# Performance work log

Measured on AMD Instinct MI355X. Metric: run time of the kernel, lower is better.

## Reference

```python
import jax, jax.numpy as jnp
import numpy as np

N = 100000   # nodes
E = 1200000  # edges
D = 64       # input_features == hidden_features
L = 3        # num_layers
EPS = 1e-5   # BatchNorm1d eps
SLOPE = 0.2  # LeakyReLU negative slope


def setup_inputs() -> dict:
    key = jax.random.key(0)
    k_x, k_e, k_w = jax.random.split(key, 3)
    x = jax.random.normal(k_x, (N, D), dtype=jnp.float32)
    edge_index = jax.random.randint(k_e, (2, E), 0, N, dtype=jnp.int32)
    # Glorot-ish linear weights per layer, stacked [L, D, D]; bias zeros.
    Ws = jax.random.normal(k_w, (L, D, D), dtype=jnp.float32) / np.float32(np.sqrt(D))
    bs = jnp.zeros((L, D), dtype=jnp.float32)
    # BatchNorm affine params (training-mode batch statistics are used).
    gammas = jnp.ones((L, D), dtype=jnp.float32)
    betas = jnp.zeros((L, D), dtype=jnp.float32)
    return {"x": x, "edge_index": edge_index, "Ws": Ws, "bs": bs,
            "gammas": gammas, "betas": betas}


def reference(x, edge_index, Ws, bs, gammas, betas):
    src, dst = edge_index[0], edge_index[1]
    # GCN symmetric normalization with self-loops: deg = in-degree + 1
    deg = jax.ops.segment_sum(jnp.ones((E,), x.dtype), dst, num_segments=N) + 1.0
    dinv = jax.lax.rsqrt(deg)
    enorm = (dinv[src] * dinv[dst])[:, None]  # [E,1] edge norm
    snorm = (dinv * dinv)[:, None]            # [N,1] self-loop norm
    for l in range(L):
        xw = x @ Ws[l]                                        # [N,D]
        agg = (jax.ops.segment_sum(xw[src] * enorm, dst, num_segments=N)
               + xw * snorm + bs[l])                          # GCNConv output
        h = jnp.where(agg > 0, agg, SLOPE * agg)              # LeakyReLU(0.2)
        mu = h.mean(axis=0)
        var = h.var(axis=0)                                   # biased var (PyTorch BN)
        x = gammas[l] * (h - mu) * jax.lax.rsqrt(var + EPS) + betas[l]
    return x
```

## Files before the change

### kernel.cpp

```cpp
#include <hip/hip_runtime.h>

#define D 64
#define SLOPE 0.2f
#define BN_EPS 1e-5f
#define BSHIFT 9
#define BUCKET 512
#define CHUNK 8192

static __device__ __forceinline__ unsigned pk_bf16(float fx, float fy) {
    unsigned bx = __float_as_uint(fx);
    unsigned by = __float_as_uint(fy);
    bx = (bx + 0x7fffu + ((bx >> 16) & 1u)) >> 16;
    by = (by + 0x7fffu + ((by >> 16) & 1u)) & 0xffff0000u;
    return bx | by;
}
static __device__ __forceinline__ float bf_lo(unsigned u) { return __uint_as_float(u << 16); }
static __device__ __forceinline__ float bf_hi(unsigned u) { return __uint_as_float(u & 0xffff0000u); }

__global__ __launch_bounds__(256) void k_hist(const int* __restrict__ dst,
                                              int* __restrict__ bcnt, int E) {
    __shared__ int hist[256];
    hist[threadIdx.x] = 0;
    __syncthreads();
    for (int e = blockIdx.x * 256 + threadIdx.x; e < E; e += gridDim.x * 256)
        atomicAdd(&hist[dst[e] >> BSHIFT], 1);
    __syncthreads();
    const int v = hist[threadIdx.x];
    if (v) atomicAdd(&bcnt[threadIdx.x], v);
}

__global__ __launch_bounds__(256) void k_bscan(const int* __restrict__ bcnt,
                                               int* __restrict__ bbase, int* __restrict__ pcur,
                                               unsigned* __restrict__ ybf, int NB, int E, int N) {
    __shared__ int l[256];
    const int t = threadIdx.x;
    const int v = (t < NB) ? bcnt[t] : 0;
    l[t] = v;
    __syncthreads();
    for (int off = 1; off < 256; off <<= 1) {
        int x = l[t];
        if (t >= off) x += l[t - off];
        __syncthreads();
        l[t] = x;
        __syncthreads();
    }
    const int excl = l[t] - v;
    if (t < NB) { bbase[t] = excl; pcur[t] = excl; }
    if (t == 0) bbase[NB] = E;
    if (t < 32) ybf[(size_t)N * 32 + t] = 0u;
}

__global__ __launch_bounds__(256) void k_part(const int* __restrict__ src,
                                              const int* __restrict__ dst,
                                              int* __restrict__ pcur,
                                              unsigned* __restrict__ arena, int E) {
    __shared__ unsigned stage[CHUNK];
    __shared__ unsigned char bktb[CHUNK];
    __shared__ int hist[256], lofs[256], gbase[256];
    const int t = threadIdx.x;
    const int e0 = blockIdx.x * CHUNK;
    const int cn = min(CHUNK, E - e0);

    hist[t] = 0;
    __syncthreads();
    for (int i = t; i < cn; i += 256)
        atomicAdd(&hist[dst[e0 + i] >> BSHIFT], 1);
    __syncthreads();
    const int v = hist[t];
    lofs[t] = v;
    __syncthreads();
    for (int off = 1; off < 256; off <<= 1) {
        int x = lofs[t];
        if (t >= off) x += lofs[t - off];
        __syncthreads();
        lofs[t] = x;
        __syncthreads();
    }
    const int excl = lofs[t] - v;
    __syncthreads();
    lofs[t] = excl;
    if (v > 0) gbase[t] = atomicAdd(&pcur[t], v);
    __syncthreads();
    for (int i = t; i < cn; i += 256) {
        const int dd = dst[e0 + i];
        const int b  = dd >> BSHIFT;
        const int p  = atomicAdd(&lofs[b], 1);
        stage[p] = ((unsigned)(dd & (BUCKET - 1)) << 23) | (unsigned)src[e0 + i];
        bktb[p]  = (unsigned char)b;
    }
    __syncthreads();
    for (int i = t; i < cn; i += 256) {
        const int b = bktb[i];
        const int startb = lofs[b] - hist[b];
        arena[gbase[b] + (i - startb)] = stage[i];
    }
}

__global__ __launch_bounds__(512) void k_build(const unsigned* __restrict__ arena,
                                               const int* __restrict__ bbase,
                                               int* __restrict__ rp, int* __restrict__ pcnt,
                                               int* __restrict__ colbuf, float* __restrict__ dinv,
                                               int N) {
    __shared__ int ncnt[512], sc[512], lcur[512];
    const int t = threadIdx.x;
    const int nbase  = blockIdx.x << BSHIFT;
    const int nlocal = min(BUCKET, N - nbase);
    const int abeg = bbase[blockIdx.x];
    const int aend = bbase[blockIdx.x + 1];
    const int pbase = abeg + 7 * nbase;

    ncnt[t] = 0;
    __syncthreads();
    for (int i = abeg + t; i < aend; i += 512)
        atomicAdd(&ncnt[arena[i] >> 23], 1);
    __syncthreads();
    const int v = ncnt[t];
    const int p = (v + 7) & ~7;
    sc[t] = p;
    __syncthreads();
    for (int off = 1; off < 512; off <<= 1) {
        int x = sc[t];
        if (t >= off) x += sc[t - off];
        __syncthreads();
        sc[t] = x;
        __syncthreads();
    }
    const int excl = sc[t] - p;
    lcur[t] = pbase + excl;
    if (t < nlocal) {
        rp[nbase + t]   = pbase + excl;
        pcnt[nbase + t] = p;
        dinv[nbase + t] = rsqrtf((float)v + 1.0f);
    }
    __syncthreads();
    for (int i = abeg + t; i < aend; i += 512) {
        const unsigned u = arena[i];
        const int pos = atomicAdd(&lcur[u >> 23], 1);
        colbuf[pos] = (int)(u & 0x7FFFFFu);
    }
    if (t < nlocal)
        for (int k = v; k < p; ++k) colbuf[pbase + excl + k] = N;
}

__global__ __launch_bounds__(256) void k_gemm(const float* __restrict__ x,
                                              const float* __restrict__ W,
                                              const float* __restrict__ stats,
                                              const float* __restrict__ gamma,
                                              const float* __restrict__ beta,
                                              const float* __restrict__ dinv,
                                              unsigned* __restrict__ ybf,
                                              float invN, int affine, int N) {
    __shared__ float scs[D], shs[D];
    const int tid = threadIdx.x;
    if (tid < D) {
        float sc = 1.f, sh = 0.f;
        if (affine) {
            const float mu  = stats[tid] * invN;
            const float var = stats[D + tid] * invN - mu * mu;
            sc = gamma[tid] * rsqrtf(var + BN_EPS);
            sh = beta[tid] - mu * sc;
        }
        scs[tid] = sc; shs[tid] = sh;
    }
    __syncthreads();

    const int lane = tid & 63;
    const int wib  = tid >> 6;
    float Wreg[D];
    float bv = 0.f;
#pragma unroll
    for (int k = 0; k < D; ++k) {
        const float w = W[k * D + lane];
        Wreg[k] = scs[k] * w;
        bv = fmaf(shs[k], w, bv);
    }
    const int stride = gridDim.x * 4;
    for (int row = __builtin_amdgcn_readfirstlane(blockIdx.x * 4 + wib); row < N; row += stride) {
        const float4* xr = (const float4*)(x + (size_t)row * D);
        float acc = 0.f;
#pragma unroll
        for (int k4 = 0; k4 < 16; ++k4) {
            const float4 xv = xr[k4];
            acc = fmaf(xv.x, Wreg[4 * k4 + 0], acc);
            acc = fmaf(xv.y, Wreg[4 * k4 + 1], acc);
            acc = fmaf(xv.z, Wreg[4 * k4 + 2], acc);
            acc = fmaf(xv.w, Wreg[4 * k4 + 3], acc);
        }
        const float r  = (acc + bv) * dinv[row];
        const float rn = __shfl_down(r, 1, 64);
        if (!(lane & 1))
            ybf[(size_t)row * 32 + (lane >> 1)] = pk_bf16(r, rn);
    }
}

__global__ __launch_bounds__(256) void k_pull(const int* __restrict__ rp,
                                              const int* __restrict__ pcnt,
                                              const int* __restrict__ colbuf,
                                              const unsigned* __restrict__ ybf,
                                              const float* __restrict__ dinv,
                                              const float* __restrict__ b,
                                              float* __restrict__ h,
                                              float* __restrict__ stats, int N) {
    const int tid  = threadIdx.x;
    const int lane = tid & 63;
    const int t32  = lane & 31;
    const int hw   = lane >> 5;
    const int wv   = tid >> 6;
    const float b0 = b[2 * t32];
    const float b1 = b[2 * t32 + 1];
    float s1a = 0.f, s1b = 0.f, s2a = 0.f, s2b = 0.f;

    const int gw = blockIdx.x * 4 + wv;
    const int gstride = gridDim.x * 4;

    for (int pr = gw; 2 * pr < N; pr += gstride) {
        const int n  = 2 * pr + hw;
        const bool vn = n < N;
        const int st = vn ? rp[n]   : 0;
        const int pd = vn ? pcnt[n] : 0;

        float a[8][2];
#pragma unroll
        for (int c = 0; c < 8; ++c) { a[c][0] = 0.f; a[c][1] = 0.f; }
        {
            const unsigned u = vn ? ybf[(size_t)n * 32 + t32] : 0u;
            a[0][0] = bf_lo(u); a[0][1] = bf_hi(u);
        }
        for (int w0 = 0; w0 < pd; w0 += 32) {
            const int wn = min(pd - w0, 32);
            const int ci = (t32 < wn) ? colbuf[st + w0 + t32] : 0;
            for (int j0 = 0; j0 < wn; j0 += 8) {
#pragma unroll
                for (int jj = 0; jj < 8; ++jj) {
                    const int idx = __shfl(ci, hw * 32 + j0 + jj, 64);
                    const unsigned u = ybf[(size_t)idx * 32 + t32];
                    a[jj][0] += bf_lo(u);
                    a[jj][1] += bf_hi(u);
                }
            }
        }
        const float v0 = ((a[0][0] + a[1][0]) + (a[2][0] + a[3][0])) +
                         ((a[4][0] + a[5][0]) + (a[6][0] + a[7][0]));
        const float v1 = ((a[0][1] + a[1][1]) + (a[2][1] + a[3][1])) +
                         ((a[4][1] + a[5][1]) + (a[6][1] + a[7][1]));
        if (vn) {
            const float di = dinv[n];
            float t0 = fmaf(di, v0, b0); t0 = t0 > 0.f ? t0 : SLOPE * t0;
            float t1 = fmaf(di, v1, b1); t1 = t1 > 0.f ? t1 : SLOPE * t1;
            *(float2*)&h[(size_t)n * D + 2 * t32] = make_float2(t0, t1);
            s1a += t0; s2a += t0 * t0;
            s1b += t1; s2b += t1 * t1;
        }
    }

    __shared__ float l1[64], l2[64];
    if (tid < 64) { l1[tid] = 0.f; l2[tid] = 0.f; }
    __syncthreads();
    atomicAdd(&l1[2 * t32],     s1a);
    atomicAdd(&l1[2 * t32 + 1], s1b);
    atomicAdd(&l2[2 * t32],     s2a);
    atomicAdd(&l2[2 * t32 + 1], s2b);
    __syncthreads();
    if (tid < 64) {
        atomicAdd(&stats[tid],      l1[tid]);
        atomicAdd(&stats[64 + tid], l2[tid]);
    }
}

__global__ __launch_bounds__(256) void k_normalize(const float* __restrict__ h,
                                                   const float* __restrict__ stats,
                                                   const float* __restrict__ gamma,
                                                   const float* __restrict__ beta,
                                                   float* __restrict__ out,
                                                   float invN, int total4) {
    const int gt = blockIdx.x * 256 + threadIdx.x;
    const int c0 = (gt * 4) & 63;
    float sc[4], sh[4];
#pragma unroll
    for (int k = 0; k < 4; ++k) {
        const int c = c0 + k;
        const float mu  = stats[c] * invN;
        const float var = stats[64 + c] * invN - mu * mu;
        sc[k] = gamma[c] * rsqrtf(var + BN_EPS);
        sh[k] = beta[c] - mu * sc[k];
    }
    const float4* h4 = (const float4*)h;
    float4* o4 = (float4*)out;
    for (int i = gt; i < total4; i += gridDim.x * 256) {
        float4 v = h4[i];
        v.x = fmaf(sc[0], v.x, sh[0]);
        v.y = fmaf(sc[1], v.y, sh[1]);
        v.z = fmaf(sc[2], v.z, sh[2]);
        v.w = fmaf(sc[3], v.w, sh[3]);
        o4[i] = v;
    }
}

extern "C" void kernel_launch(void* const* d_in, const int* in_sizes, int n_in,
                              void* d_out, int out_size, void* d_ws, size_t ws_size,
                              hipStream_t stream) {
    const float* x0     = (const float*)d_in[0];
    const int*   ei     = (const int*)d_in[1];
    const float* Ws     = (const float*)d_in[2];
    const float* bs     = (const float*)d_in[3];
    const float* gammas = (const float*)d_in[4];
    const float* betas  = (const float*)d_in[5];

    const int N = in_sizes[0] / D;
    const int E = in_sizes[1] / 2;
    const int L = in_sizes[2] / (D * D);
    const int NB = (N + BUCKET - 1) >> BSHIFT;
    const int nchunks = (E + CHUNK - 1) / CHUNK;

    const int* srcp = ei;
    const int* dstp = ei + E;

    char* wsb = (char*)d_ws;
    size_t o = 0;
    auto alloc = [&](size_t elems) { size_t r = o; o += (elems + 255) & ~(size_t)255; return r; };
    const size_t o_bcnt  = alloc(256);
    const size_t o_stats = alloc((size_t)L * 128);
    const size_t zero_end = o;
    const size_t o_bbase = alloc(257);
    const size_t o_pcur  = alloc(256);
    const size_t o_rp    = alloc((size_t)N);
    const size_t o_pcnt  = alloc((size_t)N);
    const size_t o_dinv  = alloc((size_t)N);
    const size_t o_arena = alloc((size_t)E);
    const size_t o_col   = alloc((size_t)E + 7 * (size_t)N + 64);
    const size_t o_y     = alloc(((size_t)N + 1) * 32);
    const size_t o_h     = alloc((size_t)N * D);

    int*      bcnt  = (int*)(wsb + o_bcnt * 4);
    float*    stats = (float*)(wsb + o_stats * 4);
    int*      bbase = (int*)(wsb + o_bbase * 4);
    int*      pcur  = (int*)(wsb + o_pcur * 4);
    int*      rp    = (int*)(wsb + o_rp * 4);
    int*      pcnt  = (int*)(wsb + o_pcnt * 4);
    float*    dinv  = (float*)(wsb + o_dinv * 4);
    unsigned* arena = (unsigned*)(wsb + o_arena * 4);
    int*      col   = (int*)(wsb + o_col * 4);
    unsigned* ybf   = (unsigned*)(wsb + o_y * 4);
    float*    h     = (float*)(wsb + o_h * 4);
    float*    out   = (float*)d_out;

    hipMemsetAsync(d_ws, 0, zero_end * 4, stream);

    k_hist <<<512, 256, 0, stream>>>(dstp, bcnt, E);
    k_bscan<<<1,   256, 0, stream>>>(bcnt, bbase, pcur, ybf, NB, E, N);
    k_part <<<nchunks, 256, 0, stream>>>(srcp, dstp, pcur, arena, E);
    k_build<<<NB,  512, 0, stream>>>(arena, bbase, rp, pcnt, col, dinv, N);

    const float invN = 1.0f / (float)N;
    const float* xin = x0;
    for (int l = 0; l < L; ++l) {
        const int pl = l ? l - 1 : 0;
        k_gemm<<<1024, 256, 0, stream>>>(xin, Ws + (size_t)l * D * D,
                                         stats + (size_t)pl * 128,
                                         gammas + (size_t)pl * D, betas + (size_t)pl * D,
                                         dinv, ybf, invN, l > 0 ? 1 : 0, N);
        k_pull<<<2048, 256, 0, stream>>>(rp, pcnt, col, ybf, dinv, bs + (size_t)l * D,
                                         h, stats + (size_t)l * 128, N);
        xin = h;
    }
    k_normalize<<<1024, 256, 0, stream>>>(h, stats + (size_t)(L - 1) * 128,
                                          gammas + (size_t)(L - 1) * D,
                                          betas + (size_t)(L - 1) * D,
                                          out, invN, N * D / 4);
}
```

Before: 407.3 us.

## Split bf16 features into column halves and use fixed-capacity buckets

The bf16 feature table is split into two column halves, each 32 bytes per row. The pull kernel makes two passes, gathering 16 lanes per node with four nodes per wave, so each pass's gathered working set is smaller and more likely to stay in cache. The histogram and scan kernels are dropped in favour of fixed-capacity per-bucket arena and column regions (CAP=7168), which removes two launches. h is written directly into the output buffer. The risk is overflow if any bucket receives more than CAP edges, and the column index list is now read twice per layer.

After: 442.5 us. 8.6% more time.

```diff
diff --git a/kernel.cpp b/kernel.cpp
--- a/kernel.cpp
+++ b/kernel.cpp
@@ -6,6 +6,8 @@
 #define BSHIFT 9
 #define BUCKET 512
 #define CHUNK 8192
+#define CAP 7168
+#define COLCAP (CAP + 7 * BUCKET)
 
 static __device__ __forceinline__ unsigned pk_bf16(float fx, float fy) {
     unsigned bx = __float_as_uint(fx);
@@ -16,39 +18,6 @@
 }
 static __device__ __forceinline__ float bf_lo(unsigned u) { return __uint_as_float(u << 16); }
 static __device__ __forceinline__ float bf_hi(unsigned u) { return __uint_as_float(u & 0xffff0000u); }
-
-__global__ __launch_bounds__(256) void k_hist(const int* __restrict__ dst,
-                                              int* __restrict__ bcnt, int E) {
-    __shared__ int hist[256];
-    hist[threadIdx.x] = 0;
-    __syncthreads();
-    for (int e = blockIdx.x * 256 + threadIdx.x; e < E; e += gridDim.x * 256)
-        atomicAdd(&hist[dst[e] >> BSHIFT], 1);
-    __syncthreads();
-    const int v = hist[threadIdx.x];
-    if (v) atomicAdd(&bcnt[threadIdx.x], v);
-}
-
-__global__ __launch_bounds__(256) void k_bscan(const int* __restrict__ bcnt,
-                                               int* __restrict__ bbase, int* __restrict__ pcur,
-                                               unsigned* __restrict__ ybf, int NB, int E, int N) {
-    __shared__ int l[256];
-    const int t = threadIdx.x;
-    const int v = (t < NB) ? bcnt[t] : 0;
-    l[t] = v;
-    __syncthreads();
-    for (int off = 1; off < 256; off <<= 1) {
-        int x = l[t];
-        if (t >= off) x += l[t - off];
-        __syncthreads();
-        l[t] = x;
-        __syncthreads();
-    }
-    const int excl = l[t] - v;
-    if (t < NB) { bbase[t] = excl; pcur[t] = excl; }
-    if (t == 0) bbase[NB] = E;
-    if (t < 32) ybf[(size_t)N * 32 + t] = 0u;
-}
 
 __global__ __launch_bounds__(256) void k_part(const int* __restrict__ src,
                                               const int* __restrict__ dst,
@@ -79,7 +48,7 @@
     const int excl = lofs[t] - v;
     __syncthreads();
     lofs[t] = excl;
-    if (v > 0) gbase[t] = atomicAdd(&pcur[t], v);
+    if (v > 0) gbase[t] = t * CAP + atomicAdd(&pcur[t], v);
     __syncthreads();
     for (int i = t; i < cn; i += 256) {
         const int dd = dst[e0 + i];
@@ -97,22 +66,26 @@
 }
 
 __global__ __launch_bounds__(512) void k_build(const unsigned* __restrict__ arena,
-                                               const int* __restrict__ bbase,
+                                               const int* __restrict__ pcur,
                                                int* __restrict__ rp, int* __restrict__ pcnt,
                                                int* __restrict__ colbuf, float* __restrict__ dinv,
-                                               int N) {
+                                               unsigned* __restrict__ ybf, int N, int HS) {
     __shared__ int ncnt[512], sc[512], lcur[512];
     const int t = threadIdx.x;
-    const int nbase  = blockIdx.x << BSHIFT;
+    const int b = blockIdx.x;
+    const int nbase  = b << BSHIFT;
     const int nlocal = min(BUCKET, N - nbase);
-    const int abeg = bbase[blockIdx.x];
-    const int aend = bbase[blockIdx.x + 1];
-    const int pbase = abeg + 7 * nbase;
+    const int count  = pcur[b];
+    const unsigned* ab = arena + (size_t)b * CAP;
+    const int colbase = b * COLCAP;
+
+    if (b == 0 && t < 32)
+        ybf[(size_t)(t >> 4) * HS + (size_t)N * 16 + (t & 15)] = 0u;
 
     ncnt[t] = 0;
     __syncthreads();
-    for (int i = abeg + t; i < aend; i += 512)
-        atomicAdd(&ncnt[arena[i] >> 23], 1);
+    for (int i = t; i < count; i += 512)
+        atomicAdd(&ncnt[ab[i] >> 23], 1);
     __syncthreads();
     const int v = ncnt[t];
     const int p = (v + 7) & ~7;
@@ -126,20 +99,20 @@
         __syncthreads();
     }
     const int excl = sc[t] - p;
-    lcur[t] = pbase + excl;
+    lcur[t] = colbase + excl;
     if (t < nlocal) {
-        rp[nbase + t]   = pbase + excl;
+        rp[nbase + t]   = colbase + excl;
         pcnt[nbase + t] = p;
         dinv[nbase + t] = rsqrtf((float)v + 1.0f);
     }
     __syncthreads();
-    for (int i = abeg + t; i < aend; i += 512) {
-        const unsigned u = arena[i];
+    for (int i = t; i < count; i += 512) {
+        const unsigned u = ab[i];
         const int pos = atomicAdd(&lcur[u >> 23], 1);
         colbuf[pos] = (int)(u & 0x7FFFFFu);
     }
     if (t < nlocal)
-        for (int k = v; k < p; ++k) colbuf[pbase + excl + k] = N;
+        for (int k = v; k < p; ++k) colbuf[colbase + excl + k] = N;
 }
 
 __global__ __launch_bounds__(256) void k_gemm(const float* __restrict__ x,
@@ -149,7 +122,7 @@
                                               const float* __restrict__ beta,
                                               const float* __restrict__ dinv,
                                               unsigned* __restrict__ ybf,
-                                              float invN, int affine, int N) {
+                                              float invN, int affine, int N, int HS) {
     __shared__ float scs[D], shs[D];
     const int tid = threadIdx.x;
     if (tid < D) {
@@ -163,9 +136,10 @@
         scs[tid] = sc; shs[tid] = sh;
     }
     __syncthreads();
-
     const int lane = tid & 63;
     const int wib  = tid >> 6;
+    const int half = lane >> 5;
+    const int sl16 = (lane >> 1) & 15;
     float Wreg[D];
     float bv = 0.f;
 #pragma unroll
@@ -189,7 +163,7 @@
         const float r  = (acc + bv) * dinv[row];
         const float rn = __shfl_down(r, 1, 64);
         if (!(lane & 1))
-            ybf[(size_t)row * 32 + (lane >> 1)] = pk_bf16(r, rn);
+            ybf[(size_t)half * HS + (size_t)row * 16 + sl16] = pk_bf16(r, rn);
     }
 }
 
@@ -200,66 +174,75 @@
                                               const float* __restrict__ dinv,
                                               const float* __restrict__ b,
                                               float* __restrict__ h,
-                                              float* __restrict__ stats, int N) {
+                                              float* __restrict__ stats, int N, int HS) {
     const int tid  = threadIdx.x;
     const int lane = tid & 63;
-    const int t32  = lane & 31;
-    const int hw   = lane >> 5;
+    const int t16  = lane & 15;
+    const int qw   = lane >> 4;
     const int wv   = tid >> 6;
-    const float b0 = b[2 * t32];
-    const float b1 = b[2 * t32 + 1];
-    float s1a = 0.f, s1b = 0.f, s2a = 0.f, s2b = 0.f;
-
-    const int gw = blockIdx.x * 4 + wv;
+    const int gw   = blockIdx.x * 4 + wv;
     const int gstride = gridDim.x * 4;
 
-    for (int pr = gw; 2 * pr < N; pr += gstride) {
-        const int n  = 2 * pr + hw;
-        const bool vn = n < N;
-        const int st = vn ? rp[n]   : 0;
-        const int pd = vn ? pcnt[n] : 0;
-
-        float a[8][2];
-#pragma unroll
-        for (int c = 0; c < 8; ++c) { a[c][0] = 0.f; a[c][1] = 0.f; }
-        {
-            const unsigned u = vn ? ybf[(size_t)n * 32 + t32] : 0u;
-            a[0][0] = bf_lo(u); a[0][1] = bf_hi(u);
-        }
-        for (int w0 = 0; w0 < pd; w0 += 32) {
-            const int wn = min(pd - w0, 32);
-            const int ci = (t32 < wn) ? colbuf[st + w0 + t32] : 0;
-            for (int j0 = 0; j0 < wn; j0 += 8) {
-#pragma unroll
-                for (int jj = 0; jj < 8; ++jj) {
-                    const int idx = __shfl(ci, hw * 32 + j0 + jj, 64);
-                    const unsigned u = ybf[(size_t)idx * 32 + t32];
-                    a[jj][0] += bf_lo(u);
-                    a[jj][1] += bf_hi(u);
+    float s1[2][2] = {{0.f, 0.f}, {0.f, 0.f}};
+    float s2[2][2] = {{0.f, 0.f}, {0.f, 0.f}};
+
+#pragma unroll
+    for (int half = 0; half < 2; ++half) {
+        const unsigned* yb = ybf + (size_t)half * HS;
+        const float b0 = b[half * 32 + 2 * t16];
+        const float b1 = b[half * 32 + 2 * t16 + 1];
+
+        for (int pr = gw; 4 * pr < N; pr += gstride) {
+            const int n  = 4 * pr + qw;
+            const bool vn = n < N;
+            const int st = vn ? rp[n]   : 0;
+            const int pd = vn ? pcnt[n] : 0;
+
+            float a[8][2];
+#pragma unroll
+            for (int c = 0; c < 8; ++c) { a[c][0] = 0.f; a[c][1] = 0.f; }
+            {
+                const unsigned u = vn ? yb[(size_t)n * 16 + t16] : 0u;
+                a[0][0] = bf_lo(u); a[0][1] = bf_hi(u);
+            }
+            for (int w0 = 0; w0 < pd; w0 += 16) {
+                const int wn = min(pd - w0, 16);
+                const int ci = (t16 < wn) ? colbuf[st + w0 + t16] : 0;
+                for (int j0 = 0; j0 < wn; j0 += 8) {
+#pragma unroll
+                    for (int jj = 0; jj < 8; ++jj) {
+                        const int idx = __shfl(ci, qw * 16 + j0 + jj, 64);
+                        const unsigned u = yb[(size_t)idx * 16 + t16];
+                        a[jj][0] += bf_lo(u);
+                        a[jj][1] += bf_hi(u);
+                    }
                 }
             }
-        }
-        const float v0 = ((a[0][0] + a[1][0]) + (a[2][0] + a[3][0])) +
-                         ((a[4][0] + a[5][0]) + (a[6][0] + a[7][0]));
-        const float v1 = ((a[0][1] + a[1][1]) + (a[2][1] + a[3][1])) +
-                         ((a[4][1] + a[5][1]) + (a[6][1] + a[7][1]));
-        if (vn) {
-            const float di = dinv[n];
-            float t0 = fmaf(di, v0, b0); t0 = t0 > 0.f ? t0 : SLOPE * t0;
-            float t1 = fmaf(di, v1, b1); t1 = t1 > 0.f ? t1 : SLOPE * t1;
-            *(float2*)&h[(size_t)n * D + 2 * t32] = make_float2(t0, t1);
-            s1a += t0; s2a += t0 * t0;
-            s1b += t1; s2b += t1 * t1;
+            const float v0 = ((a[0][0] + a[1][0]) + (a[2][0] + a[3][0])) +
+                             ((a[4][0] + a[5][0]) + (a[6][0] + a[7][0]));
+            const float v1 = ((a[0][1] + a[1][1]) + (a[2][1] + a[3][1])) +
+                             ((a[4][1] + a[5][1]) + (a[6][1] + a[7][1]));
+            if (vn) {
+                const float di = dinv[n];
+                float t0 = fmaf(di, v0, b0); t0 = t0 > 0.f ? t0 : SLOPE * t0;
+                float t1 = fmaf(di, v1, b1); t1 = t1 > 0.f ? t1 : SLOPE * t1;
+                *(float2*)&h[(size_t)n * D + half * 32 + 2 * t16] = make_float2(t0, t1);
+                s1[half][0] += t0; s2[half][0] += t0 * t0;
+                s1[half][1] += t1; s2[half][1] += t1 * t1;
+            }
         }
     }
 
     __shared__ float l1[64], l2[64];
     if (tid < 64) { l1[tid] = 0.f; l2[tid] = 0.f; }
     __syncthreads();
-    atomicAdd(&l1[2 * t32],     s1a);
-    atomicAdd(&l1[2 * t32 + 1], s1b);
-    atomicAdd(&l2[2 * t32],     s2a);
-    atomicAdd(&l2[2 * t32 + 1], s2b);
+#pragma unroll
+    for (int half = 0; half < 2; ++half) {
+        atomicAdd(&l1[half * 32 + 2 * t16],     s1[half][0]);
+        atomicAdd(&l1[half * 32 + 2 * t16 + 1], s1[half][1]);
+        atomicAdd(&l2[half * 32 + 2 * t16],     s2[half][0]);
+        atomicAdd(&l2[half * 32 + 2 * t16 + 1], s2[half][1]);
+    }
     __syncthreads();
     if (tid < 64) {
         atomicAdd(&stats[tid],      l1[tid]);
@@ -309,8 +292,9 @@
     const int N = in_sizes[0] / D;
     const int E = in_sizes[1] / 2;
     const int L = in_sizes[2] / (D * D);
+    const int nchunks = (E + CHUNK - 1) / CHUNK;
     const int NB = (N + BUCKET - 1) >> BSHIFT;
-    const int nchunks = (E + CHUNK - 1) / CHUNK;
+    const int HS = (N + 1) * 16;
 
     const int* srcp = ei;
     const int* dstp = ei + E;
@@ -318,38 +302,31 @@
     char* wsb = (char*)d_ws;
     size_t o = 0;
     auto alloc = [&](size_t elems) { size_t r = o; o += (elems + 255) & ~(size_t)255; return r; };
-    const size_t o_bcnt  = alloc(256);
+    const size_t o_pcur  = alloc(256);
     const size_t o_stats = alloc((size_t)L * 128);
     const size_t zero_end = o;
-    const size_t o_bbase = alloc(257);
-    const size_t o_pcur  = alloc(256);
     const size_t o_rp    = alloc((size_t)N);
     const size_t o_pcnt  = alloc((size_t)N);
     const size_t o_dinv  = alloc((size_t)N);
-    const size_t o_arena = alloc((size_t)E);
-    const size_t o_col   = alloc((size_t)E + 7 * (size_t)N + 64);
-    const size_t o_y     = alloc(((size_t)N + 1) * 32);
-    const size_t o_h     = alloc((size_t)N * D);
-
-    int*      bcnt  = (int*)(wsb + o_bcnt * 4);
+    const size_t o_arena = alloc((size_t)NB * CAP);
+    const size_t o_col   = alloc((size_t)NB * COLCAP);
+    const size_t o_y     = alloc((size_t)2 * HS);
+
+    int*      pcur  = (int*)(wsb + o_pcur * 4);
     float*    stats = (float*)(wsb + o_stats * 4);
-    int*      bbase = (int*)(wsb + o_bbase * 4);
-    int*      pcur  = (int*)(wsb + o_pcur * 4);
     int*      rp    = (int*)(wsb + o_rp * 4);
     int*      pcnt  = (int*)(wsb + o_pcnt * 4);
     float*    dinv  = (float*)(wsb + o_dinv * 4);
     unsigned* arena = (unsigned*)(wsb + o_arena * 4);
     int*      col   = (int*)(wsb + o_col * 4);
     unsigned* ybf   = (unsigned*)(wsb + o_y * 4);
-    float*    h     = (float*)(wsb + o_h * 4);
     float*    out   = (float*)d_out;
+    float*    h     = out;
 
     hipMemsetAsync(d_ws, 0, zero_end * 4, stream);
 
-    k_hist <<<512, 256, 0, stream>>>(dstp, bcnt, E);
-    k_bscan<<<1,   256, 0, stream>>>(bcnt, bbase, pcur, ybf, NB, E, N);
     k_part <<<nchunks, 256, 0, stream>>>(srcp, dstp, pcur, arena, E);
-    k_build<<<NB,  512, 0, stream>>>(arena, bbase, rp, pcnt, col, dinv, N);
+    k_build<<<NB, 512, 0, stream>>>(arena, pcur, rp, pcnt, col, dinv, ybf, N, HS);
 
     const float invN = 1.0f / (float)N;
     const float* xin = x0;
@@ -358,9 +335,10 @@
         k_gemm<<<1024, 256, 0, stream>>>(xin, Ws + (size_t)l * D * D,
                                          stats + (size_t)pl * 128,
                                          gammas + (size_t)pl * D, betas + (size_t)pl * D,
-                                         dinv, ybf, invN, l > 0 ? 1 : 0, N);
-        k_pull<<<2048, 256, 0, stream>>>(rp, pcnt, col, ybf, dinv, bs + (size_t)l * D,
-                                         h, stats + (size_t)l * 128, N);
+                                         dinv, ybf, invN, l > 0 ? 1 : 0, N, HS);
+        k_pull<<<2048, 256, 0, stream>>>(rp, pcnt, col, ybf, dinv,
+                                         bs + (size_t)l * D, h,
+                                         stats + (size_t)l * 128, N, HS);
         xin = h;
     }
     k_normalize<<<1024, 256, 0, stream>>>(h, stats + (size_t)(L - 1) * 128,
```
